# Kernel tuning notes

Measured on AMD Instinct MI355X. Metric: run time of the kernel, lower is better.

The kernel has to match this reference:

```python
import jax, jax.numpy as jnp
import numpy as np

NF, NLOC, NNEI = 4, 2048, 64
EMBED, PAIR_DIM, H = 128, 64, 8
HD = EMBED // H
EPS = 1e-5

def _ln(x, g, b):
    m = x.mean(-1, keepdims=True)
    v = ((x - m) ** 2).mean(-1, keepdims=True)
    return (x - m) * jax.lax.rsqrt(v + EPS) * g + b

def setup_inputs() -> dict:
    key = jax.random.key(0)
    ks = jax.random.split(key, 12)
    inp = {
        "query": jax.random.normal(ks[0], (NF, NLOC, EMBED), jnp.float32),
        "pair": jax.random.normal(ks[1], (NF, NLOC, NNEI, PAIR_DIM), jnp.float32),
        "nlist": jax.random.randint(ks[2], (NF, NLOC, NNEI), 0, NLOC, jnp.int64),
        "delta_pos": jax.random.normal(ks[3], (NF, NLOC, NNEI, 3), jnp.float32),
        "attn_mask": jnp.zeros((NF, H, NLOC, NNEI), jnp.float32),
        "ln_g": jnp.ones((EMBED,), jnp.float32),
        "ln_b": jnp.zeros((EMBED,), jnp.float32),
        "pn_g": jnp.ones((PAIR_DIM,), jnp.float32),
        "pn_b": jnp.zeros((PAIR_DIM,), jnp.float32),
        "Wq": jax.random.normal(ks[4], (EMBED, EMBED), jnp.float32) * (EMBED ** -0.5),
        "Wk": jax.random.normal(ks[5], (EMBED, EMBED), jnp.float32) * (EMBED ** -0.5),
        "Wv": jax.random.normal(ks[6], (EMBED, EMBED), jnp.float32) * (EMBED ** -0.5),
        "Wbias": jax.random.normal(ks[7], (H, PAIR_DIM), jnp.float32) * (PAIR_DIM ** -0.5),
        "bbias": jnp.zeros((H,), jnp.float32),
        "Wforce": jax.random.normal(ks[8], (1, EMBED), jnp.float32) * (EMBED ** -0.5),
    }
    return inp

def reference(query, pair, nlist, delta_pos, attn_mask,
              ln_g, ln_b, pn_g, pn_b, Wq, Wk, Wv, Wbias, bbias, Wforce):
    nf, nloc, _ = query.shape
    nnei = nlist.shape[-1]
    qn = _ln(query, ln_g, ln_b)            # [f,l,e]
    pn = _ln(pair, pn_g, pn_b)             # [f,l,n,p]
    scaling = HD ** -0.5
    q = (qn @ Wq.T).reshape(nf, nloc, H, HD) * scaling       # [f,l,h,d]
    k = qn @ Wk.T                                            # [f,l,e]
    v = qn @ Wv.T
    idx = nlist.reshape(nf, -1)[..., None]                   # [f,l*n,1]
    kg = jnp.take_along_axis(k, idx, axis=1).reshape(nf, nloc, nnei, H, HD)
    vg = jnp.take_along_axis(v, idx, axis=1).reshape(nf, nloc, nnei, H, HD)
    attn = jnp.einsum('flhd,flnhd->fhln', q, kg)             # [f,h,l,n]
    bias = jnp.einsum('flnp,hp->fhln', pn, Wbias) + bbias[None, :, None, None]
    probs = jax.nn.softmax(attn + attn_mask + bias, axis=-1)  # dropout off (eval)
    # rotate by delta_pos and contract with v over neighbors
    x = jnp.einsum('fhln,flnc,flnhd->flchd', probs, delta_pos, vg)
    x = x.reshape(nf, nloc, 3, EMBED)
    force = (x @ Wforce.T).squeeze(-1)                       # [f,l,3]
    return force
```

## Files before the change

### kernel.cpp

```cpp
#include <hip/hip_runtime.h>

#define NFR   4
#define NLOCC 2048
#define NNEIN 64
#define EMB   128
#define PDIM  64
#define NH    8
#define LNEPS 1e-5f
#define NROW  (NFR*NLOCC)

#define WS_Q   0
#define WS_K   (NROW*EMB)
#define WS_FV  (2*NROW*EMB)

__device__ __forceinline__ void fma4(float4& acc, const float4 a, const float4 b) {
    acc.x = fmaf(a.x, b.x, acc.x);
    acc.y = fmaf(a.y, b.y, acc.y);
    acc.z = fmaf(a.z, b.z, acc.z);
    acc.w = fmaf(a.w, b.w, acc.w);
}
__device__ __forceinline__ void fma4s(float4& acc, const float s, const float4 b) {
    acc.x = fmaf(s, b.x, acc.x);
    acc.y = fmaf(s, b.y, acc.y);
    acc.z = fmaf(s, b.z, acc.z);
    acc.w = fmaf(s, b.w, acc.w);
}
__device__ __forceinline__ float hsum4(const float4 a) {
    return (a.x + a.y) + (a.z + a.w);
}
__device__ __forceinline__ float dot4(const float4 a, const float4 b) {
    return fmaf(a.x, b.x, fmaf(a.y, b.y, fmaf(a.z, b.z, a.w * b.w)));
}
__device__ __forceinline__ float4 scale4(const float4 a, const float s) {
    return make_float4(a.x*s, a.y*s, a.z*s, a.w*s);
}

__global__ __launch_bounds__(256, 2) void qkfv_kernel(
    const float* __restrict__ query,
    const float* __restrict__ ln_g, const float* __restrict__ ln_b,
    const float* __restrict__ Wq, const float* __restrict__ Wk,
    const float* __restrict__ Wv, const float* __restrict__ Wforce,
    float* __restrict__ ws)
{
    __shared__ float  gb_s[2][EMB];
    __shared__ float  qn_s[16*132];
    __shared__ float  wt_s[2][16*132];
    __shared__ float4 wvf_s4[8*33];
    const int t = threadIdx.x;
    const int rowbase = blockIdx.x * 16;

    if (t < 64) {
        const float* src = (t < 32) ? ln_g : ln_b;
        ((float4*)gb_s[t >> 5])[t & 31] = ((const float4*)src)[t & 31];
    }

    {
        const int h = t >> 5, ch = t & 31;
        float4 acc = make_float4(0.f, 0.f, 0.f, 0.f);
        #pragma unroll
        for (int d = 0; d < 16; ++d) {
            const float wf = Wforce[h*16 + d];
            const float4 wv = ((const float4*)(Wv + (size_t)(h*16 + d)*EMB))[ch];
            fma4s(acc, wf, wv);
        }
        wvf_s4[h*33 + ch] = acc;
    }

    const int r   = t >> 4;
    const int seg = t & 15;
    float4 x0 = ((const float4*)query)[(size_t)(rowbase + r)*32 + seg*2 + 0];
    float4 x1 = ((const float4*)query)[(size_t)(rowbase + r)*32 + seg*2 + 1];
    float s  = (x0.x + x0.y) + (x0.z + x0.w) + (x1.x + x1.y) + (x1.z + x1.w);
    float ss = x0.x*x0.x + x0.y*x0.y + x0.z*x0.z + x0.w*x0.w
             + x1.x*x1.x + x1.y*x1.y + x1.z*x1.z + x1.w*x1.w;
    #pragma unroll
    for (int m = 1; m < 16; m <<= 1) {
        s  += __shfl_xor(s,  m, 64);
        ss += __shfl_xor(ss, m, 64);
    }
    const float mean = s * (1.0f / 128.0f);
    const float var  = ss * (1.0f / 128.0f) - mean * mean;
    const float rstd = rsqrtf(var + LNEPS);
    __syncthreads();

    {
        const int c0 = seg * 8;
        float4 o0, o1;
        o0.x = (x0.x - mean)*rstd*gb_s[0][c0+0] + gb_s[1][c0+0];
        o0.y = (x0.y - mean)*rstd*gb_s[0][c0+1] + gb_s[1][c0+1];
        o0.z = (x0.z - mean)*rstd*gb_s[0][c0+2] + gb_s[1][c0+2];
        o0.w = (x0.w - mean)*rstd*gb_s[0][c0+3] + gb_s[1][c0+3];
        o1.x = (x1.x - mean)*rstd*gb_s[0][c0+4] + gb_s[1][c0+4];
        o1.y = (x1.y - mean)*rstd*gb_s[0][c0+5] + gb_s[1][c0+5];
        o1.z = (x1.z - mean)*rstd*gb_s[0][c0+6] + gb_s[1][c0+6];
        o1.w = (x1.w - mean)*rstd*gb_s[0][c0+7] + gb_s[1][c0+7];
        ((float4*)qn_s)[r*33 + seg*2 + 0] = o0;
        ((float4*)qn_s)[r*33 + seg*2 + 1] = o1;
    }
    __syncthreads();

    const int rp = t >> 5;
    const int r0 = rp * 2;
    const int cq = t & 31;
    const int sc0 = t >> 2;
    const int si0 = t & 3;
    const float4* qn4 = (const float4*)qn_s;

    for (int w = 0; w < 2; ++w) {
        const float4* W4 = (const float4*)((w == 0) ? Wq : Wk);
        float4 acc0 = make_float4(0.f,0.f,0.f,0.f);
        float4 acc1 = make_float4(0.f,0.f,0.f,0.f);
        {
            float4 g0 = W4[(size_t)sc0*32 + si0];
            float4 g1 = W4[(size_t)(sc0+64)*32 + si0];
            float* wt = wt_s[0];
            wt[(si0*4+0)*132 + sc0] = g0.x; wt[(si0*4+1)*132 + sc0] = g0.y;
            wt[(si0*4+2)*132 + sc0] = g0.z; wt[(si0*4+3)*132 + sc0] = g0.w;
            wt[(si0*4+0)*132 + sc0+64] = g1.x; wt[(si0*4+1)*132 + sc0+64] = g1.y;
            wt[(si0*4+2)*132 + sc0+64] = g1.z; wt[(si0*4+3)*132 + sc0+64] = g1.w;
        }
        __syncthreads();
        #pragma unroll
        for (int tau = 0; tau < 8; ++tau) {
            const int buf = tau & 1;
            float4 ng0, ng1;
            if (tau < 7) {
                ng0 = W4[(size_t)sc0*32 + (tau+1)*4 + si0];
                ng1 = W4[(size_t)(sc0+64)*32 + (tau+1)*4 + si0];
            }
            const float4* wt4 = (const float4*)wt_s[buf];
            #pragma unroll
            for (int e4 = 0; e4 < 4; ++e4) {
                float4 a0 = qn4[r0*33 + tau*4 + e4];
                float4 a1 = qn4[(r0+1)*33 + tau*4 + e4];
                const float* a0p = (const float*)&a0;
                const float* a1p = (const float*)&a1;
                #pragma unroll
                for (int ee = 0; ee < 4; ++ee) {
                    const float4 wv = wt4[(e4*4+ee)*33 + cq];
                    fma4s(acc0, a0p[ee], wv);
                    fma4s(acc1, a1p[ee], wv);
                }
            }
            if (tau < 7) {
                float* wt = wt_s[buf ^ 1];
                wt[(si0*4+0)*132 + sc0] = ng0.x; wt[(si0*4+1)*132 + sc0] = ng0.y;
                wt[(si0*4+2)*132 + sc0] = ng0.z; wt[(si0*4+3)*132 + sc0] = ng0.w;
                wt[(si0*4+0)*132 + sc0+64] = ng1.x; wt[(si0*4+1)*132 + sc0+64] = ng1.y;
                wt[(si0*4+2)*132 + sc0+64] = ng1.z; wt[(si0*4+3)*132 + sc0+64] = ng1.w;
            }
            __syncthreads();
        }
        const float sc = (w == 0) ? 0.25f : 1.0f;
        float4* dst = (float4*)(ws + (w == 0 ? WS_Q : WS_K));
        dst[(size_t)(rowbase + r0)*32 + cq]     = scale4(acc0, sc);
        dst[(size_t)(rowbase + r0 + 1)*32 + cq] = scale4(acc1, sc);
    }

    if (t < 128) {
        const int rr = t >> 3, h = t & 7;
        float4 acc = make_float4(0.f,0.f,0.f,0.f);
        #pragma unroll
        for (int ch = 0; ch < 32; ++ch)
            fma4(acc, qn4[rr*33 + ch], wvf_s4[h*33 + ch]);
        ws[WS_FV + (size_t)(rowbase + rr)*NH + h] = hsum4(acc);
    }
}

__global__ __launch_bounds__(256, 4) void attn_force_kernel(
    const float* __restrict__ pair, const int* __restrict__ nlist,
    const float* __restrict__ delta_pos, const float* __restrict__ attn_mask,
    const float* __restrict__ pn_g, const float* __restrict__ pn_b,
    const float* __restrict__ Wbias, const float* __restrict__ bbias,
    const float* __restrict__ ws, float* __restrict__ out)
{
    __shared__ float4 pair_s4[64*17];
    __shared__ float  logit_s[NNEIN*9];
    __shared__ float4 G_s4[128];
    __shared__ float  csg_s[16];
    __shared__ float  fv_s[NNEIN*9];
    __shared__ float  dp_s[192];
    __shared__ float  fpart[4][3];

    const int t    = threadIdx.x;
    const int bid  = blockIdx.x;
    const int fr   = bid >> 11;
    const int l    = bid & 2047;
    const int w    = t >> 6;
    const int lane = t & 63;
    const int half = lane >> 5;
    const int c    = lane & 31;
    const int n    = t >> 2;
    const int sub  = t & 3;
    const int h0   = sub * 2, h1 = h0 + 1;
    const int i32  = lane & 31;
    const int hh   = t >> 5;

    {
        const float4* p4 = (const float4*)pair + (size_t)bid*1024;
        #pragma unroll
        for (int i = 0; i < 4; ++i) {
            const int ci   = i*256 + t;
            const float4 v = p4[ci];
            pair_s4[(ci >> 4)*17 + (ci & 15)] = v;
        }
    }
    const int jv = nlist[(size_t)bid*NNEIN + lane];
    const float4 q4c = ((const float4*)(ws + WS_Q))[(size_t)bid*32 + c];

    const float mask0 = attn_mask[((size_t)(fr*NH + h0)*NLOCC + l)*NNEIN + n];
    const float mask1 = attn_mask[((size_t)(fr*NH + h1)*NLOCC + l)*NNEIN + n];

    if (t < 128) {
        const int p4i = t & 15;
        const float4 wb4 = ((const float4*)Wbias)[t];
        const float4 pg4 = ((const float4*)pn_g)[p4i];
        G_s4[t] = make_float4(wb4.x*pg4.x, wb4.y*pg4.y, wb4.z*pg4.z, wb4.w*pg4.w);
    } else if (t < 192) {
        const int h = (t - 128) >> 3, s8 = (t - 128) & 7;
        float sg = 0.f, cb = 0.f;
        #pragma unroll
        for (int k = 0; k < 8; ++k) {
            const int p = s8*8 + k;
            const float wb = Wbias[h*PDIM + p];
            sg = fmaf(pn_g[p], wb, sg);
            cb = fmaf(pn_b[p], wb, cb);
        }
        sg += __shfl_xor(sg, 1, 64); sg += __shfl_xor(sg, 2, 64); sg += __shfl_xor(sg, 4, 64);
        cb += __shfl_xor(cb, 1, 64); cb += __shfl_xor(cb, 2, 64); cb += __shfl_xor(cb, 4, 64);
        if (s8 == 0) { csg_s[h] = sg; csg_s[8 + h] = cb + bbias[h]; }
    } else if (t < 240) {
        ((float4*)dp_s)[t - 192] = ((const float4*)(delta_pos + (size_t)bid*192))[t - 192];
    }

    {
        const int    jn  = __shfl(jv, n & 63, 64);
        const float2 fv2 = ((const float2*)(ws + WS_FV + ((size_t)(fr << 11) + jn)*NH))[sub];
        fv_s[n*9 + h0] = fv2.x;
        fv_s[n*9 + h1] = fv2.y;
    }

    {
        const float4* k4 = (const float4*)(ws + WS_K) + (size_t)(fr << 11)*32;
        int jr[8];
        #pragma unroll
        for (int i = 0; i < 8; ++i)
            jr[i] = __shfl(jv, (w << 4) | (i << 1) | half, 64);
        float4 kkA[4], kkB[4];
        #pragma unroll
        for (int i = 0; i < 4; ++i) kkA[i] = k4[(size_t)jr[i]*32 + c];
        #pragma unroll
        for (int i = 0; i < 4; ++i) kkB[i] = k4[(size_t)jr[4+i]*32 + c];
        float p[8];
        #pragma unroll
        for (int i = 0; i < 4; ++i) p[i]     = dot4(kkA[i], q4c);
        #pragma unroll
        for (int i = 0; i < 4; ++i) p[4 + i] = dot4(kkB[i], q4c);
        #pragma unroll
        for (int i = 0; i < 8; ++i) {
            float pp = p[i];
            pp += __shfl_xor(pp, 1, 64);
            pp += __shfl_xor(pp, 2, 64);
            if ((c & 3) == 0)
                logit_s[((w << 4) | (i << 1) | half)*9 + (c >> 2)] = pp;
        }
    }
    __syncthreads();

    {
        const float4 pr0 = pair_s4[n*17 + sub*4 + 0];
        const float4 pr1 = pair_s4[n*17 + sub*4 + 1];
        const float4 pr2 = pair_s4[n*17 + sub*4 + 2];
        const float4 pr3 = pair_s4[n*17 + sub*4 + 3];
        float s  = hsum4(pr0) + hsum4(pr1) + hsum4(pr2) + hsum4(pr3);
        float ss = dot4(pr0, pr0) + dot4(pr1, pr1) + dot4(pr2, pr2) + dot4(pr3, pr3);
        s  += __shfl_xor(s, 1, 64);  s  += __shfl_xor(s, 2, 64);
        ss += __shfl_xor(ss, 1, 64); ss += __shfl_xor(ss, 2, 64);
        const float mean = s * (1.0f / 64.0f);
        const float var  = ss * (1.0f / 64.0f) - mean * mean;
        const float rstd = rsqrtf(var + LNEPS);

        float d[NH];
        #pragma unroll
        for (int h = 0; h < NH; ++h) d[h] = 0.f;
        const float4 prq[4] = {pr0, pr1, pr2, pr3};
        #pragma unroll
        for (int q = 0; q < 4; ++q) {
            #pragma unroll
            for (int h = 0; h < NH; ++h)
                d[h] += dot4(prq[q], G_s4[h*16 + sub*4 + q]);
        }
        #pragma unroll
        for (int h = 0; h < NH; ++h) {
            d[h] += __shfl_xor(d[h], 1, 64);
            d[h] += __shfl_xor(d[h], 2, 64);
        }
        logit_s[n*9 + h0] += rstd*(d[h0] - mean*csg_s[h0]) + csg_s[8 + h0] + mask0;
        logit_s[n*9 + h1] += rstd*(d[h1] - mean*csg_s[h1]) + csg_s[8 + h1] + mask1;
    }
    __syncthreads();

    {
        const float a = logit_s[i32*9 + hh], b = logit_s[(i32 + 32)*9 + hh];
        float m = fmaxf(a, b);
        #pragma unroll
        for (int mm = 16; mm >= 1; mm >>= 1) m = fmaxf(m, __shfl_xor(m, mm, 64));
        const float ea = __expf(a - m), eb = __expf(b - m);
        float sum = ea + eb;
        #pragma unroll
        for (int mm = 16; mm >= 1; mm >>= 1) sum += __shfl_xor(sum, mm, 64);
        const float inv = 1.0f / sum;
        float ca = ea * inv * fv_s[i32*9 + hh];
        float cb = eb * inv * fv_s[(i32 + 32)*9 + hh];
        ca += __shfl_xor(ca, 32, 64);
        cb += __shfl_xor(cb, 32, 64);
        const float dpax = dp_s[i32*3 + 0],        dpay = dp_s[i32*3 + 1],        dpaz = dp_s[i32*3 + 2];
        const float dpbx = dp_s[(i32+32)*3 + 0],   dpby = dp_s[(i32+32)*3 + 1],   dpbz = dp_s[(i32+32)*3 + 2];
        float f0 = ca*dpax + cb*dpbx;
        float f1 = ca*dpay + cb*dpby;
        float f2 = ca*dpaz + cb*dpbz;
        #pragma unroll
        for (int mm = 1; mm <= 16; mm <<= 1) {
            f0 += __shfl_xor(f0, mm, 64);
            f1 += __shfl_xor(f1, mm, 64);
            f2 += __shfl_xor(f2, mm, 64);
        }
        if (lane == 0) {
            fpart[w][0] = f0; fpart[w][1] = f1; fpart[w][2] = f2;
        }
    }
    __syncthreads();

    if (t < 3)
        out[(size_t)bid*3 + t] = fpart[0][t] + fpart[1][t] + fpart[2][t] + fpart[3][t];
}

extern "C" void kernel_launch(void* const* d_in, const int* in_sizes, int n_in,
                              void* d_out, int out_size, void* d_ws, size_t ws_size,
                              hipStream_t stream) {
    const float* query     = (const float*)d_in[0];
    const float* pair      = (const float*)d_in[1];
    const int*   nlist     = (const int*)d_in[2];
    const float* delta_pos = (const float*)d_in[3];
    const float* attn_mask = (const float*)d_in[4];
    const float* ln_g      = (const float*)d_in[5];
    const float* ln_b      = (const float*)d_in[6];
    const float* pn_g      = (const float*)d_in[7];
    const float* pn_b      = (const float*)d_in[8];
    const float* Wq        = (const float*)d_in[9];
    const float* Wk        = (const float*)d_in[10];
    const float* Wv        = (const float*)d_in[11];
    const float* Wbias     = (const float*)d_in[12];
    const float* bbias     = (const float*)d_in[13];
    const float* Wforce    = (const float*)d_in[14];
    float* out = (float*)d_out;
    float* ws  = (float*)d_ws;

    qkfv_kernel<<<512, 256, 0, stream>>>(query, ln_g, ln_b, Wq, Wk, Wv, Wforce, ws);
    attn_force_kernel<<<NROW, 256, 0, stream>>>(pair, nlist, delta_pos, attn_mask,
                                                pn_g, pn_b, Wbias, bbias, ws, out);
}
```

Baseline: 254.9 us.

## Map one wavefront per row and one lane per neighbor in attention kernel

The attention/force kernel now handles four rows per block, with one wavefront per row and one lane per neighbor. Each lane streams its own pair vector, gathered key row, fv values and delta_pos directly from global memory. This removes most shared-memory staging and all but one intra-block barrier, and softmax and force reduction are done with wave shuffles. The pair-norm bias constants (Wbias scaled by pn_g, plus the summed gain and bias terms) are now computed once by block 0 of the first kernel and stored in the workspace, instead of in every block. In exchange, per-lane strided loads of pair and K rows are less coalesced, and a block-index swizzle is added to spread rows across blocks.

```diff
diff --git a/kernel.cpp b/kernel.cpp
--- a/kernel.cpp
+++ b/kernel.cpp
@@ -12,6 +12,7 @@
 #define WS_Q   0
 #define WS_K   (NROW*EMB)
 #define WS_FV  (2*NROW*EMB)
+#define WS_G   (2*NROW*EMB + NROW*NH)
 
 __device__ __forceinline__ void fma4(float4& acc, const float4 a, const float4 b) {
     acc.x = fmaf(a.x, b.x, acc.x);
@@ -40,6 +41,8 @@
     const float* __restrict__ ln_g, const float* __restrict__ ln_b,
     const float* __restrict__ Wq, const float* __restrict__ Wk,
     const float* __restrict__ Wv, const float* __restrict__ Wforce,
+    const float* __restrict__ pn_g, const float* __restrict__ pn_b,
+    const float* __restrict__ Wbias, const float* __restrict__ bbias,
     float* __restrict__ ws)
 {
     __shared__ float  gb_s[2][EMB];
@@ -52,6 +55,31 @@
     if (t < 64) {
         const float* src = (t < 32) ? ln_g : ln_b;
         ((float4*)gb_s[t >> 5])[t & 31] = ((const float4*)src)[t & 31];
+    }
+
+    if (blockIdx.x == 0) {
+        if (t < 128) {
+            const float4 wb4 = ((const float4*)Wbias)[t];
+            const float4 pg4 = ((const float4*)pn_g)[t & 15];
+            ((float4*)(ws + WS_G))[t] =
+                make_float4(wb4.x*pg4.x, wb4.y*pg4.y, wb4.z*pg4.z, wb4.w*pg4.w);
+        } else if (t < 192) {
+            const int h = (t - 128) >> 3, s8 = (t - 128) & 7;
+            float sg = 0.f, cb = 0.f;
+            #pragma unroll
+            for (int k = 0; k < 8; ++k) {
+                const int p = s8*8 + k;
+                const float wb = Wbias[h*PDIM + p];
+                sg = fmaf(pn_g[p], wb, sg);
+                cb = fmaf(pn_b[p], wb, cb);
+            }
+            sg += __shfl_xor(sg, 1, 64); sg += __shfl_xor(sg, 2, 64); sg += __shfl_xor(sg, 4, 64);
+            cb += __shfl_xor(cb, 1, 64); cb += __shfl_xor(cb, 2, 64); cb += __shfl_xor(cb, 4, 64);
+            if (s8 == 0) {
+                ws[WS_G + 512 + h] = sg;
+                ws[WS_G + 520 + h] = cb + bbias[h];
+            }
+        }
     }
 
     {
@@ -167,172 +195,95 @@
     }
 }
 
-__global__ __launch_bounds__(256, 4) void attn_force_kernel(
+__global__ __launch_bounds__(256, 8) void attn_force_kernel(
     const float* __restrict__ pair, const int* __restrict__ nlist,
     const float* __restrict__ delta_pos, const float* __restrict__ attn_mask,
-    const float* __restrict__ pn_g, const float* __restrict__ pn_b,
-    const float* __restrict__ Wbias, const float* __restrict__ bbias,
     const float* __restrict__ ws, float* __restrict__ out)
 {
-    __shared__ float4 pair_s4[64*17];
-    __shared__ float  logit_s[NNEIN*9];
-    __shared__ float4 G_s4[128];
-    __shared__ float  csg_s[16];
-    __shared__ float  fv_s[NNEIN*9];
-    __shared__ float  dp_s[192];
-    __shared__ float  fpart[4][3];
+    __shared__ float4 q_s4[4*32];
 
     const int t    = threadIdx.x;
-    const int bid  = blockIdx.x;
-    const int fr   = bid >> 11;
-    const int l    = bid & 2047;
     const int w    = t >> 6;
     const int lane = t & 63;
-    const int half = lane >> 5;
-    const int c    = lane & 31;
-    const int n    = t >> 2;
-    const int sub  = t & 3;
-    const int h0   = sub * 2, h1 = h0 + 1;
-    const int i32  = lane & 31;
-    const int hh   = t >> 5;
-
-    {
-        const float4* p4 = (const float4*)pair + (size_t)bid*1024;
-        #pragma unroll
-        for (int i = 0; i < 4; ++i) {
-            const int ci   = i*256 + t;
-            const float4 v = p4[ci];
-            pair_s4[(ci >> 4)*17 + (ci & 15)] = v;
-        }
-    }
-    const int jv = nlist[(size_t)bid*NNEIN + lane];
-    const float4 q4c = ((const float4*)(ws + WS_Q))[(size_t)bid*32 + c];
-
-    const float mask0 = attn_mask[((size_t)(fr*NH + h0)*NLOCC + l)*NNEIN + n];
-    const float mask1 = attn_mask[((size_t)(fr*NH + h1)*NLOCC + l)*NNEIN + n];
-
-    if (t < 128) {
-        const int p4i = t & 15;
-        const float4 wb4 = ((const float4*)Wbias)[t];
-        const float4 pg4 = ((const float4*)pn_g)[p4i];
-        G_s4[t] = make_float4(wb4.x*pg4.x, wb4.y*pg4.y, wb4.z*pg4.z, wb4.w*pg4.w);
-    } else if (t < 192) {
-        const int h = (t - 128) >> 3, s8 = (t - 128) & 7;
-        float sg = 0.f, cb = 0.f;
-        #pragma unroll
-        for (int k = 0; k < 8; ++k) {
-            const int p = s8*8 + k;
-            const float wb = Wbias[h*PDIM + p];
-            sg = fmaf(pn_g[p], wb, sg);
-            cb = fmaf(pn_b[p], wb, cb);
-        }
-        sg += __shfl_xor(sg, 1, 64); sg += __shfl_xor(sg, 2, 64); sg += __shfl_xor(sg, 4, 64);
-        cb += __shfl_xor(cb, 1, 64); cb += __shfl_xor(cb, 2, 64); cb += __shfl_xor(cb, 4, 64);
-        if (s8 == 0) { csg_s[h] = sg; csg_s[8 + h] = cb + bbias[h]; }
-    } else if (t < 240) {
-        ((float4*)dp_s)[t - 192] = ((const float4*)(delta_pos + (size_t)bid*192))[t - 192];
-    }
-
-    {
-        const int    jn  = __shfl(jv, n & 63, 64);
-        const float2 fv2 = ((const float2*)(ws + WS_FV + ((size_t)(fr << 11) + jn)*NH))[sub];
-        fv_s[n*9 + h0] = fv2.x;
-        fv_s[n*9 + h1] = fv2.y;
-    }
-
-    {
-        const float4* k4 = (const float4*)(ws + WS_K) + (size_t)(fr << 11)*32;
-        int jr[8];
-        #pragma unroll
-        for (int i = 0; i < 8; ++i)
-            jr[i] = __shfl(jv, (w << 4) | (i << 1) | half, 64);
-        float4 kkA[4], kkB[4];
-        #pragma unroll
-        for (int i = 0; i < 4; ++i) kkA[i] = k4[(size_t)jr[i]*32 + c];
-        #pragma unroll
-        for (int i = 0; i < 4; ++i) kkB[i] = k4[(size_t)jr[4+i]*32 + c];
-        float p[8];
-        #pragma unroll
-        for (int i = 0; i < 4; ++i) p[i]     = dot4(kkA[i], q4c);
-        #pragma unroll
-        for (int i = 0; i < 4; ++i) p[4 + i] = dot4(kkB[i], q4c);
-        #pragma unroll
-        for (int i = 0; i < 8; ++i) {
-            float pp = p[i];
-            pp += __shfl_xor(pp, 1, 64);
-            pp += __shfl_xor(pp, 2, 64);
-            if ((c & 3) == 0)
-                logit_s[((w << 4) | (i << 1) | half)*9 + (c >> 2)] = pp;
-        }
-    }
-    __syncthreads();
-
-    {
-        const float4 pr0 = pair_s4[n*17 + sub*4 + 0];
-        const float4 pr1 = pair_s4[n*17 + sub*4 + 1];
-        const float4 pr2 = pair_s4[n*17 + sub*4 + 2];
-        const float4 pr3 = pair_s4[n*17 + sub*4 + 3];
-        float s  = hsum4(pr0) + hsum4(pr1) + hsum4(pr2) + hsum4(pr3);
-        float ss = dot4(pr0, pr0) + dot4(pr1, pr1) + dot4(pr2, pr2) + dot4(pr3, pr3);
-        s  += __shfl_xor(s, 1, 64);  s  += __shfl_xor(s, 2, 64);
-        ss += __shfl_xor(ss, 1, 64); ss += __shfl_xor(ss, 2, 64);
-        const float mean = s * (1.0f / 64.0f);
-        const float var  = ss * (1.0f / 64.0f) - mean * mean;
-        const float rstd = rsqrtf(var + LNEPS);
-
-        float d[NH];
-        #pragma unroll
-        for (int h = 0; h < NH; ++h) d[h] = 0.f;
-        const float4 prq[4] = {pr0, pr1, pr2, pr3};
-        #pragma unroll
-        for (int q = 0; q < 4; ++q) {
-            #pragma unroll
-            for (int h = 0; h < NH; ++h)
-                d[h] += dot4(prq[q], G_s4[h*16 + sub*4 + q]);
-        }
-        #pragma unroll
-        for (int h = 0; h < NH; ++h) {
-            d[h] += __shfl_xor(d[h], 1, 64);
-            d[h] += __shfl_xor(d[h], 2, 64);
-        }
-        logit_s[n*9 + h0] += rstd*(d[h0] - mean*csg_s[h0]) + csg_s[8 + h0] + mask0;
-        logit_s[n*9 + h1] += rstd*(d[h1] - mean*csg_s[h1]) + csg_s[8 + h1] + mask1;
-    }
-    __syncthreads();
-
-    {
-        const float a = logit_s[i32*9 + hh], b = logit_s[(i32 + 32)*9 + hh];
-        float m = fmaxf(a, b);
-        #pragma unroll
-        for (int mm = 16; mm >= 1; mm >>= 1) m = fmaxf(m, __shfl_xor(m, mm, 64));
-        const float ea = __expf(a - m), eb = __expf(b - m);
-        float sum = ea + eb;
-        #pragma unroll
-        for (int mm = 16; mm >= 1; mm >>= 1) sum += __shfl_xor(sum, mm, 64);
-        const float inv = 1.0f / sum;
-        float ca = ea * inv * fv_s[i32*9 + hh];
-        float cb = eb * inv * fv_s[(i32 + 32)*9 + hh];
-        ca += __shfl_xor(ca, 32, 64);
-        cb += __shfl_xor(cb, 32, 64);
-        const float dpax = dp_s[i32*3 + 0],        dpay = dp_s[i32*3 + 1],        dpaz = dp_s[i32*3 + 2];
-        const float dpbx = dp_s[(i32+32)*3 + 0],   dpby = dp_s[(i32+32)*3 + 1],   dpbz = dp_s[(i32+32)*3 + 2];
-        float f0 = ca*dpax + cb*dpbx;
-        float f1 = ca*dpay + cb*dpby;
-        float f2 = ca*dpaz + cb*dpbz;
-        #pragma unroll
-        for (int mm = 1; mm <= 16; mm <<= 1) {
-            f0 += __shfl_xor(f0, mm, 64);
-            f1 += __shfl_xor(f1, mm, 64);
-            f2 += __shfl_xor(f2, mm, 64);
-        }
-        if (lane == 0) {
-            fpart[w][0] = f0; fpart[w][1] = f1; fpart[w][2] = f2;
-        }
-    }
-    __syncthreads();
-
-    if (t < 3)
-        out[(size_t)bid*3 + t] = fpart[0][t] + fpart[1][t] + fpart[2][t] + fpart[3][t];
+    const int bid  = ((blockIdx.x & 7) << 8) | (blockIdx.x >> 3);
+    const int row  = (bid << 2) | w;
+    const int fr   = row >> 11;
+    const int l    = row & (NLOCC - 1);
+    const int n    = lane;
+
+    if (lane < 32)
+        q_s4[(w << 5) | lane] = ((const float4*)(ws + WS_Q))[(size_t)row*32 + lane];
+
+    const int jn = nlist[(size_t)row*NNEIN + n];
+
+    const float* dpp = delta_pos + ((size_t)row*NNEIN + n)*3;
+    const float dpx = dpp[0], dpy = dpp[1], dpz = dpp[2];
+
+    const float4* pr4 = (const float4*)(pair + ((size_t)row*NNEIN + n)*PDIM);
+    const float4* Gg  = (const float4*)(ws + WS_G);
+    float d[NH];
+    #pragma unroll
+    for (int h = 0; h < NH; ++h) d[h] = 0.f;
+    float s = 0.f, ss = 0.f;
+    #pragma unroll 4
+    for (int c4 = 0; c4 < 16; ++c4) {
+        const float4 p4 = pr4[c4];
+        s  += hsum4(p4);
+        ss += dot4(p4, p4);
+        #pragma unroll
+        for (int h = 0; h < NH; ++h)
+            d[h] += dot4(p4, Gg[h*16 + c4]);
+    }
+    const float mean = s * (1.0f / 64.0f);
+    const float var  = ss * (1.0f / 64.0f) - mean * mean;
+    const float rstd = rsqrtf(var + LNEPS);
+
+    float qk[NH];
+    #pragma unroll
+    for (int h = 0; h < NH; ++h) qk[h] = 0.f;
+    const float4* k4   = (const float4*)(ws + WS_K) + ((size_t)(fr << 11) + jn)*32;
+    const float4* qrow = &q_s4[w << 5];
+    #pragma unroll 4
+    for (int c4 = 0; c4 < 32; ++c4)
+        qk[c4 >> 2] += dot4(k4[c4], qrow[c4]);
+
+    const float* SGp = ws + WS_G + 512;
+    float lg[NH];
+    #pragma unroll
+    for (int h = 0; h < NH; ++h)
+        lg[h] = qk[h] + rstd*(d[h] - mean*SGp[h]) + SGp[8 + h]
+              + attn_mask[(((size_t)(fr*NH + h))*NLOCC + l)*NNEIN + n];
+
+    const float4* fvp = (const float4*)(ws + WS_FV + ((size_t)(fr << 11) + jn)*NH);
+    const float4 fa = fvp[0];
+    const float4 fb = fvp[1];
+
+    float p[NH];
+    #pragma unroll
+    for (int h = 0; h < NH; ++h) {
+        float m = lg[h];
+        #pragma unroll
+        for (int mm = 1; mm < 64; mm <<= 1)
+            m = fmaxf(m, __shfl_xor(m, mm, 64));
+        const float e = __expf(lg[h] - m);
+        float sum = e;
+        #pragma unroll
+        for (int mm = 1; mm < 64; mm <<= 1)
+            sum += __shfl_xor(sum, mm, 64);
+        p[h] = e * (1.0f / sum);
+    }
+
+    const float sn = p[0]*fa.x + p[1]*fa.y + p[2]*fa.z + p[3]*fa.w
+                   + p[4]*fb.x + p[5]*fb.y + p[6]*fb.z + p[7]*fb.w;
+    float f0 = sn*dpx, f1 = sn*dpy, f2 = sn*dpz;
+    #pragma unroll
+    for (int mm = 1; mm < 64; mm <<= 1) {
+        f0 += __shfl_xor(f0, mm, 64);
+        f1 += __shfl_xor(f1, mm, 64);
+        f2 += __shfl_xor(f2, mm, 64);
+    }
+    if (lane < 3)
+        out[(size_t)row*3 + lane] = (lane == 0) ? f0 : ((lane == 1) ? f1 : f2);
 }
 
 extern "C" void kernel_launch(void* const* d_in, const int* in_sizes, int n_in,
@@ -356,7 +307,8 @@
     float* out = (float*)d_out;
     float* ws  = (float*)d_ws;
 
-    qkfv_kernel<<<512, 256, 0, stream>>>(query, ln_g, ln_b, Wq, Wk, Wv, Wforce, ws);
-    attn_force_kernel<<<NROW, 256, 0, stream>>>(pair, nlist, delta_pos, attn_mask,
-                                                pn_g, pn_b, Wbias, bbias, ws, out);
-}
+    qkfv_kernel<<<512, 256, 0, stream>>>(query, ln_g, ln_b, Wq, Wk, Wv, Wforce,
+                                         pn_g, pn_b, Wbias, bbias, ws);
+    attn_force_kernel<<<NROW/4, 256, 0, stream>>>(pair, nlist, delta_pos, attn_mask,
+                                                  ws, out);
+}
```

Result: slower. 301.6 us (+18.3%).

## Precompute pair-bias weights once and load pair rows directly into registers

Applied to the files above, without the earlier changes.

The folded pair-norm/bias weights (Wbias*pn_g and the per-head constants) are now computed once by block 0 of the first kernel and stored in the workspace, instead of being recomputed in every attention block. The attention kernel reads pair rows straight into registers rather than staging them through shared memory, and computes the bias into a separate shared buffer before the same barrier as the q·k logits. This removes one __syncthreads and the pair shared-memory buffer. The mask loads are now coalesced per head. Costs are more live registers per thread and a per-wave replicated copy of the weights in shared memory.

```diff
diff --git a/kernel.cpp b/kernel.cpp
--- a/kernel.cpp
+++ b/kernel.cpp
@@ -12,6 +12,7 @@
 #define WS_Q   0
 #define WS_K   (NROW*EMB)
 #define WS_FV  (2*NROW*EMB)
+#define WS_G   (2*NROW*EMB + NROW*NH)
 
 __device__ __forceinline__ void fma4(float4& acc, const float4 a, const float4 b) {
     acc.x = fmaf(a.x, b.x, acc.x);
@@ -40,6 +41,8 @@
     const float* __restrict__ ln_g, const float* __restrict__ ln_b,
     const float* __restrict__ Wq, const float* __restrict__ Wk,
     const float* __restrict__ Wv, const float* __restrict__ Wforce,
+    const float* __restrict__ pn_g, const float* __restrict__ pn_b,
+    const float* __restrict__ Wbias, const float* __restrict__ bbias,
     float* __restrict__ ws)
 {
     __shared__ float  gb_s[2][EMB];
@@ -52,6 +55,31 @@
     if (t < 64) {
         const float* src = (t < 32) ? ln_g : ln_b;
         ((float4*)gb_s[t >> 5])[t & 31] = ((const float4*)src)[t & 31];
+    }
+
+    if (blockIdx.x == 0) {
+        if (t < 128) {
+            const float4 wb4 = ((const float4*)Wbias)[t];
+            const float4 pg4 = ((const float4*)pn_g)[t & 15];
+            ((float4*)(ws + WS_G))[t] =
+                make_float4(wb4.x*pg4.x, wb4.y*pg4.y, wb4.z*pg4.z, wb4.w*pg4.w);
+        } else if (t < 192) {
+            const int h = (t - 128) >> 3, s8 = (t - 128) & 7;
+            float sg = 0.f, cb = 0.f;
+            #pragma unroll
+            for (int k = 0; k < 8; ++k) {
+                const int p = s8*8 + k;
+                const float wb = Wbias[h*PDIM + p];
+                sg = fmaf(pn_g[p], wb, sg);
+                cb = fmaf(pn_b[p], wb, cb);
+            }
+            sg += __shfl_xor(sg, 1, 64); sg += __shfl_xor(sg, 2, 64); sg += __shfl_xor(sg, 4, 64);
+            cb += __shfl_xor(cb, 1, 64); cb += __shfl_xor(cb, 2, 64); cb += __shfl_xor(cb, 4, 64);
+            if (s8 == 0) {
+                ws[WS_G + 512 + h] = sg;
+                ws[WS_G + 520 + h] = cb + bbias[h];
+            }
+        }
     }
 
     {
@@ -170,95 +198,101 @@
 __global__ __launch_bounds__(256, 4) void attn_force_kernel(
     const float* __restrict__ pair, const int* __restrict__ nlist,
     const float* __restrict__ delta_pos, const float* __restrict__ attn_mask,
-    const float* __restrict__ pn_g, const float* __restrict__ pn_b,
-    const float* __restrict__ Wbias, const float* __restrict__ bbias,
     const float* __restrict__ ws, float* __restrict__ out)
 {
-    __shared__ float4 pair_s4[64*17];
     __shared__ float  logit_s[NNEIN*9];
-    __shared__ float4 G_s4[128];
-    __shared__ float  csg_s[16];
+    __shared__ float  bias_s[NNEIN*9];
     __shared__ float  fv_s[NNEIN*9];
     __shared__ float  dp_s[192];
+    __shared__ float4 gw_s4[4*128];
     __shared__ float  fpart[4][3];
 
     const int t    = threadIdx.x;
     const int bid  = blockIdx.x;
     const int fr   = bid >> 11;
-    const int l    = bid & 2047;
+    const int l    = bid & (NLOCC - 1);
     const int w    = t >> 6;
     const int lane = t & 63;
+    const int n    = t >> 2;
+    const int sub  = t & 3;
     const int half = lane >> 5;
     const int c    = lane & 31;
-    const int n    = t >> 2;
-    const int sub  = t & 3;
-    const int h0   = sub * 2, h1 = h0 + 1;
+    const int hh   = t >> 5;
     const int i32  = lane & 31;
-    const int hh   = t >> 5;
-
-    {
-        const float4* p4 = (const float4*)pair + (size_t)bid*1024;
-        #pragma unroll
-        for (int i = 0; i < 4; ++i) {
-            const int ci   = i*256 + t;
-            const float4 v = p4[ci];
-            pair_s4[(ci >> 4)*17 + (ci & 15)] = v;
-        }
-    }
+
     const int jv = nlist[(size_t)bid*NNEIN + lane];
+
     const float4 q4c = ((const float4*)(ws + WS_Q))[(size_t)bid*32 + c];
 
-    const float mask0 = attn_mask[((size_t)(fr*NH + h0)*NLOCC + l)*NNEIN + n];
-    const float mask1 = attn_mask[((size_t)(fr*NH + h1)*NLOCC + l)*NNEIN + n];
-
-    if (t < 128) {
-        const int p4i = t & 15;
-        const float4 wb4 = ((const float4*)Wbias)[t];
-        const float4 pg4 = ((const float4*)pn_g)[p4i];
-        G_s4[t] = make_float4(wb4.x*pg4.x, wb4.y*pg4.y, wb4.z*pg4.z, wb4.w*pg4.w);
-    } else if (t < 192) {
-        const int h = (t - 128) >> 3, s8 = (t - 128) & 7;
-        float sg = 0.f, cb = 0.f;
-        #pragma unroll
-        for (int k = 0; k < 8; ++k) {
-            const int p = s8*8 + k;
-            const float wb = Wbias[h*PDIM + p];
-            sg = fmaf(pn_g[p], wb, sg);
-            cb = fmaf(pn_b[p], wb, cb);
-        }
-        sg += __shfl_xor(sg, 1, 64); sg += __shfl_xor(sg, 2, 64); sg += __shfl_xor(sg, 4, 64);
-        cb += __shfl_xor(cb, 1, 64); cb += __shfl_xor(cb, 2, 64); cb += __shfl_xor(cb, 4, 64);
-        if (s8 == 0) { csg_s[h] = sg; csg_s[8 + h] = cb + bbias[h]; }
-    } else if (t < 240) {
+    const size_t mbase = (((size_t)(fr*NH + hh))*NLOCC + l)*NNEIN;
+    const float ma = attn_mask[mbase + i32];
+    const float mb = attn_mask[mbase + i32 + 32];
+
+    const float4* pr4 = (const float4*)(pair + ((size_t)bid*NNEIN + n)*PDIM) + sub*4;
+    const float4 p0 = pr4[0];
+    const float4 p1 = pr4[1];
+    const float4 p2 = pr4[2];
+    const float4 p3 = pr4[3];
+
+    {
+        const float4* Gg = (const float4*)(ws + WS_G);
+        gw_s4[(w << 7) | lane]        = Gg[lane];
+        gw_s4[(w << 7) | (64 + lane)] = Gg[64 + lane];
+    }
+
+    if (t >= 192 && t < 240)
         ((float4*)dp_s)[t - 192] = ((const float4*)(delta_pos + (size_t)bid*192))[t - 192];
-    }
-
-    {
-        const int    jn  = __shfl(jv, n & 63, 64);
+
+    int jr[8];
+    #pragma unroll
+    for (int i = 0; i < 8; ++i)
+        jr[i] = __shfl(jv, (w << 4) | (i << 1) | half, 64);
+    const float4* k4 = (const float4*)(ws + WS_K) + (size_t)(fr << 11)*32;
+    float4 kk[8];
+    #pragma unroll
+    for (int i = 0; i < 8; ++i) kk[i] = k4[(size_t)jr[i]*32 + c];
+
+    {
+        const int jn = __shfl(jv, n & 63, 64);
         const float2 fv2 = ((const float2*)(ws + WS_FV + ((size_t)(fr << 11) + jn)*NH))[sub];
-        fv_s[n*9 + h0] = fv2.x;
-        fv_s[n*9 + h1] = fv2.y;
-    }
-
-    {
-        const float4* k4 = (const float4*)(ws + WS_K) + (size_t)(fr << 11)*32;
-        int jr[8];
-        #pragma unroll
-        for (int i = 0; i < 8; ++i)
-            jr[i] = __shfl(jv, (w << 4) | (i << 1) | half, 64);
-        float4 kkA[4], kkB[4];
-        #pragma unroll
-        for (int i = 0; i < 4; ++i) kkA[i] = k4[(size_t)jr[i]*32 + c];
-        #pragma unroll
-        for (int i = 0; i < 4; ++i) kkB[i] = k4[(size_t)jr[4+i]*32 + c];
-        float p[8];
-        #pragma unroll
-        for (int i = 0; i < 4; ++i) p[i]     = dot4(kkA[i], q4c);
-        #pragma unroll
-        for (int i = 0; i < 4; ++i) p[4 + i] = dot4(kkB[i], q4c);
+        fv_s[n*9 + sub*2]     = fv2.x;
+        fv_s[n*9 + sub*2 + 1] = fv2.y;
+    }
+
+    {
+        float s  = hsum4(p0) + hsum4(p1) + hsum4(p2) + hsum4(p3);
+        float ss = dot4(p0,p0) + dot4(p1,p1) + dot4(p2,p2) + dot4(p3,p3);
+        float d[NH];
+        #pragma unroll
+        for (int h = 0; h < NH; ++h) d[h] = 0.f;
+        const float4* gw = &gw_s4[w << 7];
+        #pragma unroll
+        for (int h = 0; h < NH; ++h) {
+            d[h] += dot4(p0, gw[h*16 + sub*4 + 0]);
+            d[h] += dot4(p1, gw[h*16 + sub*4 + 1]);
+            d[h] += dot4(p2, gw[h*16 + sub*4 + 2]);
+            d[h] += dot4(p3, gw[h*16 + sub*4 + 3]);
+        }
+        s  += __shfl_xor(s, 1, 64);  s  += __shfl_xor(s, 2, 64);
+        ss += __shfl_xor(ss, 1, 64); ss += __shfl_xor(ss, 2, 64);
+        #pragma unroll
+        for (int h = 0; h < NH; ++h) {
+            d[h] += __shfl_xor(d[h], 1, 64);
+            d[h] += __shfl_xor(d[h], 2, 64);
+        }
+        const float mean = s * (1.0f / 64.0f);
+        const float var  = ss * (1.0f / 64.0f) - mean * mean;
+        const float rstd = rsqrtf(var + LNEPS);
+        const float* SGp = ws + WS_G + 512;
+        const int h0 = sub*2, h1 = h0 + 1;
+        bias_s[n*9 + h0] = rstd*(d[h0] - mean*SGp[h0]) + SGp[8 + h0];
+        bias_s[n*9 + h1] = rstd*(d[h1] - mean*SGp[h1]) + SGp[8 + h1];
+    }
+
+    {
         #pragma unroll
         for (int i = 0; i < 8; ++i) {
-            float pp = p[i];
+            float pp = dot4(kk[i], q4c);
             pp += __shfl_xor(pp, 1, 64);
             pp += __shfl_xor(pp, 2, 64);
             if ((c & 3) == 0)
@@ -268,40 +302,8 @@
     __syncthreads();
 
     {
-        const float4 pr0 = pair_s4[n*17 + sub*4 + 0];
-        const float4 pr1 = pair_s4[n*17 + sub*4 + 1];
-        const float4 pr2 = pair_s4[n*17 + sub*4 + 2];
-        const float4 pr3 = pair_s4[n*17 + sub*4 + 3];
-        float s  = hsum4(pr0) + hsum4(pr1) + hsum4(pr2) + hsum4(pr3);
-        float ss = dot4(pr0, pr0) + dot4(pr1, pr1) + dot4(pr2, pr2) + dot4(pr3, pr3);
-        s  += __shfl_xor(s, 1, 64);  s  += __shfl_xor(s, 2, 64);
-        ss += __shfl_xor(ss, 1, 64); ss += __shfl_xor(ss, 2, 64);
-        const float mean = s * (1.0f / 64.0f);
-        const float var  = ss * (1.0f / 64.0f) - mean * mean;
-        const float rstd = rsqrtf(var + LNEPS);
-
-        float d[NH];
-        #pragma unroll
-        for (int h = 0; h < NH; ++h) d[h] = 0.f;
-        const float4 prq[4] = {pr0, pr1, pr2, pr3};
-        #pragma unroll
-        for (int q = 0; q < 4; ++q) {
-            #pragma unroll
-            for (int h = 0; h < NH; ++h)
-                d[h] += dot4(prq[q], G_s4[h*16 + sub*4 + q]);
-        }
-        #pragma unroll
-        for (int h = 0; h < NH; ++h) {
-            d[h] += __shfl_xor(d[h], 1, 64);
-            d[h] += __shfl_xor(d[h], 2, 64);
-        }
-        logit_s[n*9 + h0] += rstd*(d[h0] - mean*csg_s[h0]) + csg_s[8 + h0] + mask0;
-        logit_s[n*9 + h1] += rstd*(d[h1] - mean*csg_s[h1]) + csg_s[8 + h1] + mask1;
-    }
-    __syncthreads();
-
-    {
-        const float a = logit_s[i32*9 + hh], b = logit_s[(i32 + 32)*9 + hh];
+        const float a = logit_s[i32*9 + hh]        + bias_s[i32*9 + hh]        + ma;
+        const float b = logit_s[(i32 + 32)*9 + hh] + bias_s[(i32 + 32)*9 + hh] + mb;
         float m = fmaxf(a, b);
         #pragma unroll
         for (int mm = 16; mm >= 1; mm >>= 1) m = fmaxf(m, __shfl_xor(m, mm, 64));
@@ -314,8 +316,8 @@
         float cb = eb * inv * fv_s[(i32 + 32)*9 + hh];
         ca += __shfl_xor(ca, 32, 64);
         cb += __shfl_xor(cb, 32, 64);
-        const float dpax = dp_s[i32*3 + 0],        dpay = dp_s[i32*3 + 1],        dpaz = dp_s[i32*3 + 2];
-        const float dpbx = dp_s[(i32+32)*3 + 0],   dpby = dp_s[(i32+32)*3 + 1],   dpbz = dp_s[(i32+32)*3 + 2];
+        const float dpax = dp_s[i32*3 + 0],      dpay = dp_s[i32*3 + 1],      dpaz = dp_s[i32*3 + 2];
+        const float dpbx = dp_s[(i32+32)*3 + 0], dpby = dp_s[(i32+32)*3 + 1], dpbz = dp_s[(i32+32)*3 + 2];
         float f0 = ca*dpax + cb*dpbx;
         float f1 = ca*dpay + cb*dpby;
         float f2 = ca*dpaz + cb*dpbz;
@@ -356,7 +358,8 @@
     float* out = (float*)d_out;
     float* ws  = (float*)d_ws;
 
-    qkfv_kernel<<<512, 256, 0, stream>>>(query, ln_g, ln_b, Wq, Wk, Wv, Wforce, ws);
+    qkfv_kernel<<<512, 256, 0, stream>>>(query, ln_g, ln_b, Wq, Wk, Wv, Wforce,
+                                         pn_g, pn_b, Wbias, bbias, ws);
     attn_force_kernel<<<NROW, 256, 0, stream>>>(pair, nlist, delta_pos, attn_mask,
-                                                pn_g, pn_b, Wbias, bbias, ws, out);
-}
+                                                ws, out);
+}
```

Measured after the change: 259.6 us. No clear change (+1.8%).
